# Optimization experiments

Measured on AMD Instinct MI355X. Metric: run time of the kernel, lower is better.

The kernel has to match this reference:

```python
import jax, jax.numpy as jnp
import numpy as np

EMB = 768
HEADS = 12
HEAD_DIM = EMB // HEADS
LN_EPS = 1e-5


def _layernorm(x, g, b):
    mu = jnp.mean(x, axis=-1, keepdims=True)
    var = jnp.mean(jnp.square(x - mu), axis=-1, keepdims=True)
    return (x - mu) * jax.lax.rsqrt(var + LN_EPS) * g + b


def _att_block(x, ln_g, ln_b, w_qkv, b_qkv, w_proj, b_proj):
    # x: [b, n, e]
    B, N, E = x.shape
    h, d = HEADS, HEAD_DIM
    qkv = _layernorm(x, ln_g, ln_b) @ w_qkv.T + b_qkv          # [b, n, 3e]
    # einops 'b n (h d qkv)': last axis factors as (h, d, 3), qkv innermost
    qkv = qkv.reshape(B, N, h, d, 3)
    qkv = jnp.moveaxis(qkv, (4, 2), (0, 2))                    # [3, b, h, n, d]
    q, k, v = qkv[0], qkv[1], qkv[2]
    scale = d ** (-0.5)
    # NOTE: original code DIVIDES by scale (= multiplies by sqrt(d)) -- faithful
    scores = jnp.einsum('bhqd,bhkd->bhqk', q, k) / scale       # [b, h, n, n]
    attn = jax.nn.softmax(scores, axis=-1)
    out = jnp.einsum('bhqk,bhkd->bhqd', attn, v)               # [b, h, n, d]
    out = out.transpose(0, 2, 1, 3).reshape(B, N, E)           # [b, n, e]
    return x + out @ w_proj.T + b_proj


def setup_inputs() -> dict:
    key = jax.random.key(0)
    ks = jax.random.split(key, 8)
    B, N, E = 2, 2048, EMB
    s = E ** (-0.5)
    return {
        'modal1': jax.random.normal(ks[0], (B, N, E), jnp.float32),
        'modal2': jax.random.normal(ks[1], (B, N, E), jnp.float32),
        'ln1_g': jnp.ones((E,), jnp.float32),
        'ln1_b': jnp.zeros((E,), jnp.float32),
        'w_qkv1': jax.random.normal(ks[2], (3 * E, E), jnp.float32) * s,
        'b_qkv1': jnp.zeros((3 * E,), jnp.float32),
        'w_proj1': jax.random.normal(ks[3], (E, E), jnp.float32) * s,
        'b_proj1': jnp.zeros((E,), jnp.float32),
        'ln2_g': jnp.ones((E,), jnp.float32),
        'ln2_b': jnp.zeros((E,), jnp.float32),
        'w_qkv2': jax.random.normal(ks[4], (3 * E, E), jnp.float32) * s,
        'b_qkv2': jnp.zeros((3 * E,), jnp.float32),
        'w_proj2': jax.random.normal(ks[5], (E, E), jnp.float32) * s,
        'b_proj2': jnp.zeros((E,), jnp.float32),
    }


def reference(modal1, modal2, ln1_g, ln1_b, w_qkv1, b_qkv1, w_proj1, b_proj1,
              ln2_g, ln2_b, w_qkv2, b_qkv2, w_proj2, b_proj2):
    out1 = _att_block(modal1, ln1_g, ln1_b, w_qkv1, b_qkv1, w_proj1, b_proj1)
    out2 = _att_block(modal2, ln2_g, ln2_b, w_qkv2, b_qkv2, w_proj2, b_proj2)
    return (out1, out2)
```

## Files before the change

### kernel.cpp

```cpp
#include <hip/hip_runtime.h>
#include <hip/hip_bf16.h>


typedef unsigned short u16;
typedef unsigned int   u32;
typedef __attribute__((ext_vector_type(4)))  float floatx4;
typedef __attribute__((ext_vector_type(16))) float floatx16;
typedef __attribute__((ext_vector_type(8)))  short shortx8;
typedef __attribute__((ext_vector_type(2)))  unsigned int uintx2;

#define EMB   768
#define SEQ   2048
#define NHEAD 12
#define HDIM  64
#define RPM   4096
#define NROW  8192
#define NUNIT 48
#define KTS   4096

__device__ __forceinline__ float bf2f(u16 h) {
  union { u32 u; float f; } v; v.u = ((u32)h) << 16; return v.f;
}
__device__ __forceinline__ u16 f2bf(float f) {
  union { float f; u32 u; } v; v.f = f;
  u32 r = v.u + 0x7fffu + ((v.u >> 16) & 1u);
  return (u16)(r >> 16);
}
__device__ __forceinline__ u32 cvtpk_bf16(float a, float b) {
  u32 r;
  asm("v_cvt_pk_bf16_f32 %0, %1, %2" : "=v"(r) : "v"(a), "v"(b));
  return r;
}
__device__ __forceinline__ void swap_halves(u32 a, u32 b, u32& x, u32& y) {
#if __has_builtin(__builtin_amdgcn_permlane32_swap)
  uintx2 r = __builtin_amdgcn_permlane32_swap(a, b, false, false);
  x = r.x; y = r.y;
#else
  u32 ax = (u32)__shfl_xor((int)a, 32);
  u32 bx = (u32)__shfl_xor((int)b, 32);
  bool h = (threadIdx.x & 32) != 0;
  x = h ? bx : a;
  y = h ? b : ax;
#endif
}

__global__ __launch_bounds__(256) void prep_wq(
    const float* __restrict__ wq1, const float* __restrict__ wq2,
    u16* __restrict__ wh, u16* __restrict__ wl)
{
  int bx = blockIdx.x;
  int modal = bx / 2304, rowp = bx % 2304;
  int typ = rowp / 768, hd = rowp % 768;
  const float* W = (modal ? wq2 : wq1) + (size_t)(hd * 3 + typ) * EMB;
  size_t dst = (size_t)bx * EMB;
  int t = threadIdx.x;
  #pragma unroll
  for (int i = 0; i < 3; ++i) {
    int e = t + i * 256;
    float v = W[e];
    u16 h = f2bf(v);
    wh[dst + e] = h;
    wl[dst + e] = f2bf(v - bf2f(h));
  }
}

__global__ __launch_bounds__(256) void prep_wp(
    const float* __restrict__ wp1, const float* __restrict__ wp2,
    u16* __restrict__ wh)
{
  int bx = blockIdx.x;
  int modal = bx / 768, row = bx % 768;
  const float* W = (modal ? wp2 : wp1) + (size_t)row * EMB;
  size_t dst = (size_t)bx * EMB;
  int t = threadIdx.x;
  #pragma unroll
  for (int i = 0; i < 3; ++i) {
    int e = t + i * 256;
    wh[dst + e] = f2bf(W[e]);
  }
}

__global__ __launch_bounds__(256) void k_ln(
    const float* __restrict__ x1, const float* __restrict__ x2,
    const float* __restrict__ g1, const float* __restrict__ b1,
    const float* __restrict__ g2, const float* __restrict__ b2,
    u16* __restrict__ xn_hi, u16* __restrict__ xn_lo)
{
  int row = blockIdx.x;
  int modal = row >> 12;
  const float* x = modal ? x2 : x1;
  const float* g = modal ? g2 : g1;
  const float* bb = modal ? b2 : b1;
  int r = row & (RPM - 1);
  const float* xr = x + (size_t)r * EMB;
  int t = threadIdx.x;
  float v0 = xr[t], v1 = xr[t + 256], v2 = xr[t + 512];
  float s = v0 + v1 + v2;
  float s2 = v0 * v0 + v1 * v1 + v2 * v2;
  #pragma unroll
  for (int m = 1; m < 64; m <<= 1) { s += __shfl_xor(s, m); s2 += __shfl_xor(s2, m); }
  __shared__ float ls[4], ls2[4];
  int w = t >> 6;
  if ((t & 63) == 0) { ls[w] = s; ls2[w] = s2; }
  __syncthreads();
  s = ls[0] + ls[1] + ls[2] + ls[3];
  s2 = ls2[0] + ls2[1] + ls2[2] + ls2[3];
  float mu = s * (1.0f / EMB);
  float var = s2 * (1.0f / EMB) - mu * mu;
  float rs = rsqrtf(var + 1e-5f);
  size_t base = (size_t)row * EMB;
  float vv[3] = { v0, v1, v2 };
  #pragma unroll
  for (int i = 0; i < 3; ++i) {
    int e = t + i * 256;
    float xn = (vv[i] - mu) * rs * g[e] + bb[e];
    u16 h = f2bf(xn);
    xn_hi[base + e] = h;
    xn_lo[base + e] = f2bf(xn - bf2f(h));
  }
}

__global__ __launch_bounds__(256) void k_qkv(
    const u16* __restrict__ xn_hi, const u16* __restrict__ xn_lo,
    const u16* __restrict__ wqh, const u16* __restrict__ wql,
    const float* __restrict__ bq1, const float* __restrict__ bq2,
    u16* __restrict__ q_hi, u16* __restrict__ q_lo,
    u16* __restrict__ k_hi, u16* __restrict__ k_lo,
    u16* __restrict__ vT)
{
  int mt = blockIdx.x, ntile = blockIdx.y, modal = blockIdx.z;
  const float* BQ = modal ? bq2 : bq1;
  int typ = ntile / 6;
  int hd0 = (ntile % 6) * 128;

  __shared__ __align__(16) u16 As_hi[128 * 32], Wh[128 * 32], As_lo[128 * 32], Wl[128 * 32];

  int tid = threadIdx.x, lane = tid & 63, w = tid >> 6;
  int wm = (w >> 1) * 64, wn = (w & 1) * 64;
  int lc = lane & 15, lq = lane >> 4;

  int srow = lane >> 2;
  int schunk = ((lane & 3) ^ (srow & 3)) << 3;

  floatx4 acc[4][4] = {};
  const u16* aH = xn_hi + (size_t)(modal * RPM + mt * 128) * EMB;
  const u16* aL = xn_lo + (size_t)(modal * RPM + mt * 128) * EMB;
  const u16* wH = wqh + (size_t)(modal * 2304 + typ * 768 + hd0) * EMB;
  const u16* wL = wql + (size_t)(modal * 2304 + typ * 768 + hd0) * EMB;

  for (int k0 = 0; k0 < EMB; k0 += 32) {
    if (typ != 2) {
      #pragma unroll
      for (int c = 0; c < 8; ++c) {
        int seg = w * 8 + c;
        int tile = seg >> 3, segin = seg & 7;
        size_t off = (size_t)(segin * 16 + srow) * EMB + k0 + schunk;
        const u16* src; u16* dstb;
        if (tile == 0)      { src = aH + off; dstb = As_hi; }
        else if (tile == 1) { src = wH + off; dstb = Wh; }
        else if (tile == 2) { src = aL + off; dstb = As_lo; }
        else                { src = wL + off; dstb = Wl; }
        __builtin_amdgcn_global_load_lds(
            (const __attribute__((address_space(1))) unsigned int*)src,
            (__attribute__((address_space(3))) unsigned int*)(dstb + segin * 512), 16, 0, 0);
      }
    } else {
      #pragma unroll
      for (int c = 0; c < 4; ++c) {
        int seg = w * 4 + c;
        int tile = seg >> 3, segin = seg & 7;
        size_t off = (size_t)(segin * 16 + srow) * EMB + k0 + schunk;
        const u16* src; u16* dstb;
        if (tile == 0) { src = aH + off; dstb = As_hi; }
        else           { src = wH + off; dstb = Wh; }
        __builtin_amdgcn_global_load_lds(
            (const __attribute__((address_space(1))) unsigned int*)src,
            (__attribute__((address_space(3))) unsigned int*)(dstb + segin * 512), 16, 0, 0);
      }
    }
    __syncthreads();

    shortx8 ah[4], al[4], whf[4], wlf[4];
    int rsw = lc & 3;
    int ca = (lq ^ rsw) << 3;
    #pragma unroll
    for (int i = 0; i < 4; ++i) {
      int ra = wm + i * 16 + lc, rw = wn + i * 16 + lc;
      ah[i]  = *(const shortx8*)&As_hi[ra * 32 + ca];
      whf[i] = *(const shortx8*)&Wh[rw * 32 + ca];
      if (typ != 2) {
        al[i]  = *(const shortx8*)&As_lo[ra * 32 + ca];
        wlf[i] = *(const shortx8*)&Wl[rw * 32 + ca];
      }
    }
    #pragma unroll
    for (int i = 0; i < 4; ++i)
      #pragma unroll
      for (int jn = 0; jn < 4; ++jn) {
        acc[i][jn] = __builtin_amdgcn_mfma_f32_16x16x32_bf16(ah[i], whf[jn], acc[i][jn], 0, 0, 0);
        if (typ != 2) {
          acc[i][jn] = __builtin_amdgcn_mfma_f32_16x16x32_bf16(al[i], whf[jn], acc[i][jn], 0, 0, 0);
          acc[i][jn] = __builtin_amdgcn_mfma_f32_16x16x32_bf16(ah[i], wlf[jn], acc[i][jn], 0, 0, 0);
        }
      }
    __syncthreads();
  }

  #pragma unroll
  for (int i = 0; i < 4; ++i) {
    int mrow0 = mt * 128 + wm + i * 16 + lq * 4;
    #pragma unroll
    for (int jn = 0; jn < 4; ++jn) {
      int colp = hd0 + wn + jn * 16 + lc;
      int h = colp >> 6, d = colp & 63;
      float bias = BQ[colp * 3 + typ];
      #pragma unroll
      for (int r = 0; r < 4; ++r) {
        int mrow = mrow0 + r;
        int b = mrow >> 11, nq = mrow & (SEQ - 1);
        int uu = modal * 24 + b * 12 + h;
        float val = acc[i][jn][r] + bias;
        if (typ == 0) {
          size_t o = ((size_t)uu * SEQ + nq) * HDIM + d;
          u16 hh = f2bf(val); q_hi[o] = hh; q_lo[o] = f2bf(val - bf2f(hh));
        } else if (typ == 1) {
          size_t o = ((size_t)uu * SEQ + nq) * HDIM + d;
          u16 hh = f2bf(val); k_hi[o] = hh; k_lo[o] = f2bf(val - bf2f(hh));
        } else {
          vT[((size_t)uu * HDIM + d) * SEQ + nq] = f2bf(val);
        }
      }
    }
  }
}

__global__ __launch_bounds__(256, 3) void k_attn(
    const u16* __restrict__ q_hi, const u16* __restrict__ q_lo,
    const u16* __restrict__ k_hi, const u16* __restrict__ k_lo,
    const u16* __restrict__ vT, u16* __restrict__ attn_out)
{
  int id = blockIdx.x + (blockIdx.y << 4);
  int xcd = id & 7, j = id >> 3;
  int u = xcd * 6 + (j >> 4);
  int qt = j & 15;

  __shared__ __align__(16) u16 lds[2][3 * KTS];

  int tid = threadIdx.x, lane = tid & 63, w = tid >> 6;
  int col = lane & 31, hi = lane >> 5;
  int swz = (col & 7) << 4;

  shortx8 qh[4], qlo[4];
  {
    size_t qb = ((size_t)u * SEQ + qt * 128 + w * 32 + col) * HDIM + hi * 8;
    #pragma unroll
    for (int s = 0; s < 4; ++s) {
      qh[s]  = *(const shortx8*)(q_hi + qb + s * 16);
      qlo[s] = *(const shortx8*)(q_lo + qb + s * 16);
    }
  }

  int lrow = lane >> 3;
  int lcol = ((lane & 7) ^ lrow) << 3;
  const u16* kh_src = k_hi + (size_t)u * SEQ * HDIM;
  const u16* kl_src = k_lo + (size_t)u * SEQ * HDIM;
  const u16* v_src  = vT  + (size_t)u * HDIM * SEQ;

  auto stage = [&](int buf, int kc) {
    #pragma unroll
    for (int c = 0; c < 6; ++c) {
      int seg = w * 6 + c;
      int tile = seg >> 3, segin = seg & 7;
      u16* dst = &lds[buf][tile * KTS + segin * 512];
      const u16* src;
      if (tile == 0)      src = kh_src + (size_t)(kc + segin * 8 + lrow) * HDIM + lcol;
      else if (tile == 1) src = kl_src + (size_t)(kc + segin * 8 + lrow) * HDIM + lcol;
      else                src = v_src  + (size_t)(segin * 8 + lrow) * SEQ + kc + lcol;
      __builtin_amdgcn_global_load_lds(
          (const __attribute__((address_space(1))) unsigned int*)src,
          (__attribute__((address_space(3))) unsigned int*)dst, 16, 0, 0);
    }
  };

  floatx16 O0 = {}, O1 = {};
  float m_r = -1e30f, lsum = 0.0f;
  const float Cs = 11.5415603271f;
  const float THR = 8.0f;

  stage(0, 0);
  __syncthreads();

  for (int t = 0; t < SEQ / 64; ++t) {
    int cur = t & 1;
    if (t + 1 < SEQ / 64) stage(cur ^ 1, (t + 1) * 64);

    const char* Kh = (const char*)&lds[cur][0];
    const char* Kl = (const char*)&lds[cur][KTS];
    const char* Vt = (const char*)&lds[cur][2 * KTS];

    floatx16 S0 = {}, S1 = {};
    __builtin_amdgcn_s_setprio(1);
    #pragma unroll
    for (int s = 0; s < 4; ++s) {
      int cb = (s * 32 + hi * 16) ^ swz;
      shortx8 kf0 = *(const shortx8*)(Kh + col * 128 + cb);
      shortx8 kl0 = *(const shortx8*)(Kl + col * 128 + cb);
      shortx8 kf1 = *(const shortx8*)(Kh + (32 + col) * 128 + cb);
      shortx8 kl1 = *(const shortx8*)(Kl + (32 + col) * 128 + cb);
      S0 = __builtin_amdgcn_mfma_f32_32x32x16_bf16(kf0, qh[s],  S0, 0, 0, 0);
      S1 = __builtin_amdgcn_mfma_f32_32x32x16_bf16(kf1, qh[s],  S1, 0, 0, 0);
      S0 = __builtin_amdgcn_mfma_f32_32x32x16_bf16(kf0, qlo[s], S0, 0, 0, 0);
      S1 = __builtin_amdgcn_mfma_f32_32x32x16_bf16(kf1, qlo[s], S1, 0, 0, 0);
      S0 = __builtin_amdgcn_mfma_f32_32x32x16_bf16(kl0, qh[s],  S0, 0, 0, 0);
      S1 = __builtin_amdgcn_mfma_f32_32x32x16_bf16(kl1, qh[s],  S1, 0, 0, 0);
    }
    __builtin_amdgcn_s_setprio(0);

    float tm[16];
    #pragma unroll
    for (int r = 0; r < 16; ++r) tm[r] = fmaxf(S0[r], S1[r]);
    #pragma unroll
    for (int st = 8; st >= 1; st >>= 1)
      #pragma unroll
      for (int i = 0; i < st; ++i) tm[i] = fmaxf(tm[i], tm[i + st]);
    float mx = tm[0] * Cs;
    mx = fmaxf(mx, __shfl_xor(mx, 32));

    if (!__all(mx <= m_r + THR)) {
      float mn = fmaxf(m_r, mx);
      float alpha = __builtin_amdgcn_exp2f(m_r - mn);
      m_r = mn;
      lsum *= alpha;
      #pragma unroll
      for (int r = 0; r < 16; ++r) {
        int qsrc = (r & 3) + 8 * (r >> 2) + 4 * hi;
        union { float f; int i; } a; a.f = alpha;
        a.i = __builtin_amdgcn_ds_bpermute(qsrc << 2, a.i);
        O0[r] *= a.f; O1[r] *= a.f;
      }
    }

    #pragma unroll
    for (int r = 0; r < 16; ++r) {
      S0[r] = __builtin_amdgcn_exp2f(fmaf(Cs, S0[r], -m_r));
      S1[r] = __builtin_amdgcn_exp2f(fmaf(Cs, S1[r], -m_r));
    }
    #pragma unroll
    for (int r = 0; r < 16; ++r) tm[r] = S0[r] + S1[r];
    #pragma unroll
    for (int st = 8; st >= 1; st >>= 1)
      #pragma unroll
      for (int i = 0; i < st; ++i) tm[i] += tm[i + st];
    lsum += tm[0];

    shortx8 pf[4];
    #pragma unroll
    for (int kt = 0; kt < 2; ++kt)
      #pragma unroll
      for (int h2 = 0; h2 < 2; ++h2) {
        floatx16 Sv = kt ? S1 : S0;
        int b0 = h2 * 8;
        u32 A = cvtpk_bf16(Sv[b0 + 0], Sv[b0 + 1]);
        u32 B = cvtpk_bf16(Sv[b0 + 2], Sv[b0 + 3]);
        u32 C = cvtpk_bf16(Sv[b0 + 4], Sv[b0 + 5]);
        u32 D = cvtpk_bf16(Sv[b0 + 6], Sv[b0 + 7]);
        u32 w0, w1, w2, w3;
        swap_halves(A, C, w0, w2);
        swap_halves(B, D, w1, w3);
        union { u32 uu[4]; shortx8 ss; } pk_;
        pk_.uu[0] = w0; pk_.uu[1] = w1; pk_.uu[2] = w2; pk_.uu[3] = w3;
        pf[kt * 2 + h2] = pk_.ss;
      }

    __builtin_amdgcn_s_setprio(1);
    #pragma unroll
    for (int ks = 0; ks < 4; ++ks) {
      int cb = (ks * 32 + hi * 16) ^ swz;
      shortx8 v0 = *(const shortx8*)(Vt + col * 128 + cb);
      shortx8 v1 = *(const shortx8*)(Vt + (32 + col) * 128 + cb);
      O0 = __builtin_amdgcn_mfma_f32_32x32x16_bf16(pf[ks], v0, O0, 0, 0, 0);
      O1 = __builtin_amdgcn_mfma_f32_32x32x16_bf16(pf[ks], v1, O1, 0, 0, 0);
    }
    __builtin_amdgcn_s_setprio(0);

    __syncthreads();
  }

  float lt = lsum + __shfl_xor(lsum, 32);
  float rl = __builtin_amdgcn_rcpf(lt);
  int modal = u / 24, b = (u / 12) & 1, h = u % 12;
  size_t obase = ((size_t)(modal * RPM + b * SEQ + qt * 128 + w * 32)) * EMB + h * 64 + col;
  #pragma unroll
  for (int r = 0; r < 16; ++r) {
    int ql_ = (r & 3) + 8 * (r >> 2) + 4 * hi;
    union { float f; int i; } a; a.f = rl;
    a.i = __builtin_amdgcn_ds_bpermute(ql_ << 2, a.i);
    size_t ob = obase + (size_t)ql_ * EMB;
    attn_out[ob]      = f2bf(O0[r] * a.f);
    attn_out[ob + 32] = f2bf(O1[r] * a.f);
  }
}

__global__ __launch_bounds__(256) void k_proj(
    const u16* __restrict__ ao, const u16* __restrict__ wph,
    const float* __restrict__ x1, const float* __restrict__ x2,
    const float* __restrict__ bp1, const float* __restrict__ bp2,
    float* __restrict__ out)
{
  int mt = blockIdx.x, ntile = blockIdx.y, modal = blockIdx.z;
  const float* BP = modal ? bp2 : bp1;
  const float* x  = modal ? x2 : x1;

  __shared__ __align__(16) u16 As[64 * 32], Ws[128 * 32];
  int tid = threadIdx.x, lane = tid & 63, w = tid >> 6;
  int wm = (w >> 1) * 32, wn = (w & 1) * 64;
  int lc = lane & 15, lq = lane >> 4;

  int srow = lane >> 2;
  int schunk = ((lane & 3) ^ (srow & 3)) << 3;

  floatx4 acc[2][4] = {};
  const u16* aP = ao  + (size_t)(modal * RPM + mt * 64) * EMB;
  const u16* wP = wph + (size_t)(modal * 768 + ntile * 128) * EMB;

  for (int k0 = 0; k0 < EMB; k0 += 32) {
    #pragma unroll
    for (int c = 0; c < 3; ++c) {
      int seg = w * 3 + c;
      const u16* src; u16* dst;
      if (seg < 4) {
        src = aP + (size_t)(seg * 16 + srow) * EMB + k0 + schunk;
        dst = As + seg * 512;
      } else {
        int s2 = seg - 4;
        src = wP + (size_t)(s2 * 16 + srow) * EMB + k0 + schunk;
        dst = Ws + s2 * 512;
      }
      __builtin_amdgcn_global_load_lds(
          (const __attribute__((address_space(1))) unsigned int*)src,
          (__attribute__((address_space(3))) unsigned int*)dst, 16, 0, 0);
    }
    __syncthreads();

    int ca = (lq ^ (lc & 3)) << 3;
    shortx8 af[2], wf[4];
    #pragma unroll
    for (int i = 0; i < 2; ++i) af[i] = *(const shortx8*)&As[(wm + i * 16 + lc) * 32 + ca];
    #pragma unroll
    for (int i = 0; i < 4; ++i) wf[i] = *(const shortx8*)&Ws[(wn + i * 16 + lc) * 32 + ca];
    #pragma unroll
    for (int i = 0; i < 2; ++i)
      #pragma unroll
      for (int jn = 0; jn < 4; ++jn)
        acc[i][jn] = __builtin_amdgcn_mfma_f32_16x16x32_bf16(af[i], wf[jn], acc[i][jn], 0, 0, 0);
    __syncthreads();
  }

  #pragma unroll
  for (int i = 0; i < 2; ++i) {
    int mrow0 = mt * 64 + wm + i * 16 + lq * 4;
    #pragma unroll
    for (int jn = 0; jn < 4; ++jn) {
      int col = ntile * 128 + wn + jn * 16 + lc;
      float bias = BP[col];
      #pragma unroll
      for (int r = 0; r < 4; ++r) {
        int mrow = mrow0 + r;
        float val = acc[i][jn][r] + bias + x[(size_t)mrow * EMB + col];
        out[((size_t)(modal * RPM + mrow)) * EMB + col] = val;
      }
    }
  }
}

extern "C" void kernel_launch(void* const* d_in, const int* in_sizes, int n_in,
                              void* d_out, int out_size, void* d_ws, size_t ws_size,
                              hipStream_t stream) {
  const float* modal1 = (const float*)d_in[0];
  const float* modal2 = (const float*)d_in[1];
  const float* ln1_g  = (const float*)d_in[2];
  const float* ln1_b  = (const float*)d_in[3];
  const float* w_qkv1 = (const float*)d_in[4];
  const float* b_qkv1 = (const float*)d_in[5];
  const float* w_proj1= (const float*)d_in[6];
  const float* b_proj1= (const float*)d_in[7];
  const float* ln2_g  = (const float*)d_in[8];
  const float* ln2_b  = (const float*)d_in[9];
  const float* w_qkv2 = (const float*)d_in[10];
  const float* b_qkv2 = (const float*)d_in[11];
  const float* w_proj2= (const float*)d_in[12];
  const float* b_proj2= (const float*)d_in[13];
  float* out = (float*)d_out;

  const size_t BUFE = (size_t)NROW * EMB;
  const size_t WQE  = (size_t)2 * 2304 * EMB;
  u16* xn_hi = (u16*)d_ws;
  u16* xn_lo = xn_hi + BUFE;
  u16* q_hi  = xn_lo + BUFE;
  u16* q_lo  = q_hi + BUFE;
  u16* k_hi  = q_lo + BUFE;
  u16* k_lo  = k_hi + BUFE;
  u16* vT    = k_lo + BUFE;
  u16* wq_h  = vT + BUFE;
  u16* wq_l  = wq_h + WQE;
  u16* attn  = xn_hi;
  u16* wp_h  = q_lo;

  prep_wq<<<4608, 256, 0, stream>>>(w_qkv1, w_qkv2, wq_h, wq_l);
  k_ln<<<NROW, 256, 0, stream>>>(modal1, modal2, ln1_g, ln1_b, ln2_g, ln2_b, xn_hi, xn_lo);
  dim3 g2(32, 18, 2);
  k_qkv<<<g2, 256, 0, stream>>>(xn_hi, xn_lo, wq_h, wq_l, b_qkv1, b_qkv2,
                                q_hi, q_lo, k_hi, k_lo, vT);
  dim3 g3(16, 48);
  k_attn<<<g3, 256, 0, stream>>>(q_hi, q_lo, k_hi, k_lo, vT, attn);
  prep_wp<<<1536, 256, 0, stream>>>(w_proj1, w_proj2, wp_h);
  dim3 g4(64, 6, 2);
  k_proj<<<g4, 256, 0, stream>>>(attn, wp_h, modal1, modal2, b_proj1, b_proj2, out);
}
```

Measured before the change: 355.5 us.

## Double-buffer QKV and proj GEMM staging; compute softmax row sums via MFMA

The QKV and output-projection GEMMs now double-buffer their LDS tiles. The next K-slice is issued with global_load_lds before the current one is computed, and partial vmcnt waits with raw barriers replace __syncthreads, so global latency overlaps MFMA work. In attention, exp2 and bf16 packing are interleaved per k-step with the PV MFMAs. The softmax denominator is accumulated by an extra MFMA against a ones vector, which removes the scalar sum reduction and the final bpermute. The cost is doubled LDS in the GEMMs (lower occupancy) and an extra MFMA per PV step, plus denominators summed from bf16-rounded probabilities.

New measurement: 387.2 us. +8.9%, slower.

```diff
diff --git a/kernel.cpp b/kernel.cpp
--- a/kernel.cpp
+++ b/kernel.cpp
@@ -133,7 +133,8 @@
   int typ = ntile / 6;
   int hd0 = (ntile % 6) * 128;
 
-  __shared__ __align__(16) u16 As_hi[128 * 32], Wh[128 * 32], As_lo[128 * 32], Wl[128 * 32];
+  __shared__ __align__(16) u16 As_hi[2][128 * 32], Wh[2][128 * 32],
+                               As_lo[2][128 * 32], Wl[2][128 * 32];
 
   int tid = threadIdx.x, lane = tid & 63, w = tid >> 6;
   int wm = (w >> 1) * 64, wn = (w & 1) * 64;
@@ -148,7 +149,7 @@
   const u16* wH = wqh + (size_t)(modal * 2304 + typ * 768 + hd0) * EMB;
   const u16* wL = wql + (size_t)(modal * 2304 + typ * 768 + hd0) * EMB;
 
-  for (int k0 = 0; k0 < EMB; k0 += 32) {
+  auto stage = [&](int buf, int k0) {
     if (typ != 2) {
       #pragma unroll
       for (int c = 0; c < 8; ++c) {
@@ -156,10 +157,10 @@
         int tile = seg >> 3, segin = seg & 7;
         size_t off = (size_t)(segin * 16 + srow) * EMB + k0 + schunk;
         const u16* src; u16* dstb;
-        if (tile == 0)      { src = aH + off; dstb = As_hi; }
-        else if (tile == 1) { src = wH + off; dstb = Wh; }
-        else if (tile == 2) { src = aL + off; dstb = As_lo; }
-        else                { src = wL + off; dstb = Wl; }
+        if (tile == 0)      { src = aH + off; dstb = &As_hi[buf][0]; }
+        else if (tile == 1) { src = wH + off; dstb = &Wh[buf][0]; }
+        else if (tile == 2) { src = aL + off; dstb = &As_lo[buf][0]; }
+        else                { src = wL + off; dstb = &Wl[buf][0]; }
         __builtin_amdgcn_global_load_lds(
             (const __attribute__((address_space(1))) unsigned int*)src,
             (__attribute__((address_space(3))) unsigned int*)(dstb + segin * 512), 16, 0, 0);
@@ -171,14 +172,29 @@
         int tile = seg >> 3, segin = seg & 7;
         size_t off = (size_t)(segin * 16 + srow) * EMB + k0 + schunk;
         const u16* src; u16* dstb;
-        if (tile == 0) { src = aH + off; dstb = As_hi; }
-        else           { src = wH + off; dstb = Wh; }
+        if (tile == 0) { src = aH + off; dstb = &As_hi[buf][0]; }
+        else           { src = wH + off; dstb = &Wh[buf][0]; }
         __builtin_amdgcn_global_load_lds(
             (const __attribute__((address_space(1))) unsigned int*)src,
             (__attribute__((address_space(3))) unsigned int*)(dstb + segin * 512), 16, 0, 0);
       }
     }
-    __syncthreads();
+  };
+
+  stage(0, 0);
+  for (int kk = 0; kk < 24; ++kk) {
+    int cur = kk & 1;
+    bool more = (kk + 1 < 24);
+    if (more) stage(cur ^ 1, (kk + 1) * 32);
+    if (typ != 2) {
+      if (more) asm volatile("s_waitcnt vmcnt(8)" ::: "memory");
+      else      asm volatile("s_waitcnt vmcnt(0)" ::: "memory");
+    } else {
+      if (more) asm volatile("s_waitcnt vmcnt(4)" ::: "memory");
+      else      asm volatile("s_waitcnt vmcnt(0)" ::: "memory");
+    }
+    __builtin_amdgcn_s_barrier();
+    __builtin_amdgcn_sched_barrier(0);
 
     shortx8 ah[4], al[4], whf[4], wlf[4];
     int rsw = lc & 3;
@@ -186,11 +202,11 @@
     #pragma unroll
     for (int i = 0; i < 4; ++i) {
       int ra = wm + i * 16 + lc, rw = wn + i * 16 + lc;
-      ah[i]  = *(const shortx8*)&As_hi[ra * 32 + ca];
-      whf[i] = *(const shortx8*)&Wh[rw * 32 + ca];
+      ah[i]  = *(const shortx8*)&As_hi[cur][ra * 32 + ca];
+      whf[i] = *(const shortx8*)&Wh[cur][rw * 32 + ca];
       if (typ != 2) {
-        al[i]  = *(const shortx8*)&As_lo[ra * 32 + ca];
-        wlf[i] = *(const shortx8*)&Wl[rw * 32 + ca];
+        al[i]  = *(const shortx8*)&As_lo[cur][ra * 32 + ca];
+        wlf[i] = *(const shortx8*)&Wl[cur][rw * 32 + ca];
       }
     }
     #pragma unroll
@@ -203,7 +219,9 @@
           acc[i][jn] = __builtin_amdgcn_mfma_f32_16x16x32_bf16(ah[i], wlf[jn], acc[i][jn], 0, 0, 0);
         }
       }
-    __syncthreads();
+    asm volatile("s_waitcnt lgkmcnt(0)" ::: "memory");
+    __builtin_amdgcn_s_barrier();
+    __builtin_amdgcn_sched_barrier(0);
   }
 
   #pragma unroll
@@ -282,8 +300,13 @@
     }
   };
 
+  shortx8 ONES;
+  #pragma unroll
+  for (int i = 0; i < 8; ++i) ONES[i] = (short)0x3F80;
+
   floatx16 O0 = {}, O1 = {};
-  float m_r = -1e30f, lsum = 0.0f;
+  floatx16 Osum = {};
+  float m_r = -1e30f;
   const float Cs = 11.5415603271f;
   const float THR = 8.0f;
 
@@ -316,88 +339,68 @@
     }
     __builtin_amdgcn_s_setprio(0);
 
-    float tm[16];
-    #pragma unroll
-    for (int r = 0; r < 16; ++r) tm[r] = fmaxf(S0[r], S1[r]);
-    #pragma unroll
-    for (int st = 8; st >= 1; st >>= 1)
-      #pragma unroll
-      for (int i = 0; i < st; ++i) tm[i] = fmaxf(tm[i], tm[i + st]);
-    float mx = tm[0] * Cs;
+    float pm[16];
+    #pragma unroll
+    for (int r = 0; r < 16; ++r) pm[r] = fmaxf(S0[r], S1[r]);
+    float g0 = fmaxf(fmaxf(pm[0],  pm[1]),  pm[2]);
+    float g1 = fmaxf(fmaxf(pm[3],  pm[4]),  pm[5]);
+    float g2 = fmaxf(fmaxf(pm[6],  pm[7]),  pm[8]);
+    float g3 = fmaxf(fmaxf(pm[9],  pm[10]), pm[11]);
+    float g4 = fmaxf(fmaxf(pm[12], pm[13]), pm[14]);
+    float mx = fmaxf(fmaxf(fmaxf(g0, g1), g2), fmaxf(fmaxf(g3, g4), pm[15])) * Cs;
     mx = fmaxf(mx, __shfl_xor(mx, 32));
 
     if (!__all(mx <= m_r + THR)) {
       float mn = fmaxf(m_r, mx);
       float alpha = __builtin_amdgcn_exp2f(m_r - mn);
       m_r = mn;
-      lsum *= alpha;
       #pragma unroll
       for (int r = 0; r < 16; ++r) {
         int qsrc = (r & 3) + 8 * (r >> 2) + 4 * hi;
         union { float f; int i; } a; a.f = alpha;
         a.i = __builtin_amdgcn_ds_bpermute(qsrc << 2, a.i);
-        O0[r] *= a.f; O1[r] *= a.f;
-      }
-    }
-
-    #pragma unroll
-    for (int r = 0; r < 16; ++r) {
-      S0[r] = __builtin_amdgcn_exp2f(fmaf(Cs, S0[r], -m_r));
-      S1[r] = __builtin_amdgcn_exp2f(fmaf(Cs, S1[r], -m_r));
-    }
-    #pragma unroll
-    for (int r = 0; r < 16; ++r) tm[r] = S0[r] + S1[r];
-    #pragma unroll
-    for (int st = 8; st >= 1; st >>= 1)
-      #pragma unroll
-      for (int i = 0; i < st; ++i) tm[i] += tm[i + st];
-    lsum += tm[0];
-
-    shortx8 pf[4];
-    #pragma unroll
-    for (int kt = 0; kt < 2; ++kt)
-      #pragma unroll
-      for (int h2 = 0; h2 < 2; ++h2) {
-        floatx16 Sv = kt ? S1 : S0;
-        int b0 = h2 * 8;
-        u32 A = cvtpk_bf16(Sv[b0 + 0], Sv[b0 + 1]);
-        u32 B = cvtpk_bf16(Sv[b0 + 2], Sv[b0 + 3]);
-        u32 C = cvtpk_bf16(Sv[b0 + 4], Sv[b0 + 5]);
-        u32 D = cvtpk_bf16(Sv[b0 + 6], Sv[b0 + 7]);
-        u32 w0, w1, w2, w3;
-        swap_halves(A, C, w0, w2);
-        swap_halves(B, D, w1, w3);
-        union { u32 uu[4]; shortx8 ss; } pk_;
-        pk_.uu[0] = w0; pk_.uu[1] = w1; pk_.uu[2] = w2; pk_.uu[3] = w3;
-        pf[kt * 2 + h2] = pk_.ss;
-      }
-
-    __builtin_amdgcn_s_setprio(1);
+        O0[r] *= a.f; O1[r] *= a.f; Osum[r] *= a.f;
+      }
+    }
+
     #pragma unroll
     for (int ks = 0; ks < 4; ++ks) {
+      const int h2 = ks & 1;
+      float ee[8];
+      #pragma unroll
+      for (int i = 0; i < 8; ++i) {
+        float sv = (ks < 2) ? S0[h2 * 8 + i] : S1[h2 * 8 + i];
+        ee[i] = __builtin_amdgcn_exp2f(fmaf(Cs, sv, -m_r));
+      }
+      u32 A = cvtpk_bf16(ee[0], ee[1]);
+      u32 B = cvtpk_bf16(ee[2], ee[3]);
+      u32 C = cvtpk_bf16(ee[4], ee[5]);
+      u32 D = cvtpk_bf16(ee[6], ee[7]);
+      u32 w0, w1, w2, w3;
+      swap_halves(A, C, w0, w2);
+      swap_halves(B, D, w1, w3);
+      union { u32 uu[4]; shortx8 ss; } pk_;
+      pk_.uu[0] = w0; pk_.uu[1] = w1; pk_.uu[2] = w2; pk_.uu[3] = w3;
       int cb = (ks * 32 + hi * 16) ^ swz;
       shortx8 v0 = *(const shortx8*)(Vt + col * 128 + cb);
       shortx8 v1 = *(const shortx8*)(Vt + (32 + col) * 128 + cb);
-      O0 = __builtin_amdgcn_mfma_f32_32x32x16_bf16(pf[ks], v0, O0, 0, 0, 0);
-      O1 = __builtin_amdgcn_mfma_f32_32x32x16_bf16(pf[ks], v1, O1, 0, 0, 0);
-    }
-    __builtin_amdgcn_s_setprio(0);
+      O0   = __builtin_amdgcn_mfma_f32_32x32x16_bf16(pk_.ss, v0,   O0,   0, 0, 0);
+      O1   = __builtin_amdgcn_mfma_f32_32x32x16_bf16(pk_.ss, v1,   O1,   0, 0, 0);
+      Osum = __builtin_amdgcn_mfma_f32_32x32x16_bf16(pk_.ss, ONES, Osum, 0, 0, 0);
+    }
 
     __syncthreads();
   }
 
-  float lt = lsum + __shfl_xor(lsum, 32);
-  float rl = __builtin_amdgcn_rcpf(lt);
   int modal = u / 24, b = (u / 12) & 1, h = u % 12;
   size_t obase = ((size_t)(modal * RPM + b * SEQ + qt * 128 + w * 32)) * EMB + h * 64 + col;
   #pragma unroll
   for (int r = 0; r < 16; ++r) {
     int ql_ = (r & 3) + 8 * (r >> 2) + 4 * hi;
-    union { float f; int i; } a; a.f = rl;
-    a.i = __builtin_amdgcn_ds_bpermute(ql_ << 2, a.i);
+    float rl = __builtin_amdgcn_rcpf(Osum[r]);
     size_t ob = obase + (size_t)ql_ * EMB;
-    attn_out[ob]      = f2bf(O0[r] * a.f);
-    attn_out[ob + 32] = f2bf(O1[r] * a.f);
+    attn_out[ob]      = f2bf(O0[r] * rl);
+    attn_out[ob + 32] = f2bf(O1[r] * rl);
   }
 }
 
@@ -411,7 +414,7 @@
   const float* BP = modal ? bp2 : bp1;
   const float* x  = modal ? x2 : x1;
 
-  __shared__ __align__(16) u16 As[64 * 32], Ws[128 * 32];
+  __shared__ __align__(16) u16 As[2][64 * 32], Ws[2][128 * 32];
   int tid = threadIdx.x, lane = tid & 63, w = tid >> 6;
   int wm = (w >> 1) * 32, wn = (w & 1) * 64;
   int lc = lane & 15, lq = lane >> 4;
@@ -423,37 +426,49 @@
   const u16* aP = ao  + (size_t)(modal * RPM + mt * 64) * EMB;
   const u16* wP = wph + (size_t)(modal * 768 + ntile * 128) * EMB;
 
-  for (int k0 = 0; k0 < EMB; k0 += 32) {
+  auto stage = [&](int buf, int k0) {
     #pragma unroll
     for (int c = 0; c < 3; ++c) {
       int seg = w * 3 + c;
       const u16* src; u16* dst;
       if (seg < 4) {
         src = aP + (size_t)(seg * 16 + srow) * EMB + k0 + schunk;
-        dst = As + seg * 512;
+        dst = &As[buf][0] + seg * 512;
       } else {
         int s2 = seg - 4;
         src = wP + (size_t)(s2 * 16 + srow) * EMB + k0 + schunk;
-        dst = Ws + s2 * 512;
+        dst = &Ws[buf][0] + s2 * 512;
       }
       __builtin_amdgcn_global_load_lds(
           (const __attribute__((address_space(1))) unsigned int*)src,
           (__attribute__((address_space(3))) unsigned int*)dst, 16, 0, 0);
     }
-    __syncthreads();
+  };
+
+  stage(0, 0);
+  for (int kk = 0; kk < 24; ++kk) {
+    int cur = kk & 1;
+    bool more = (kk + 1 < 24);
+    if (more) stage(cur ^ 1, (kk + 1) * 32);
+    if (more) asm volatile("s_waitcnt vmcnt(3)" ::: "memory");
+    else      asm volatile("s_waitcnt vmcnt(0)" ::: "memory");
+    __builtin_amdgcn_s_barrier();
+    __builtin_amdgcn_sched_barrier(0);
 
     int ca = (lq ^ (lc & 3)) << 3;
     shortx8 af[2], wf[4];
     #pragma unroll
-    for (int i = 0; i < 2; ++i) af[i] = *(const shortx8*)&As[(wm + i * 16 + lc) * 32 + ca];
-    #pragma unroll
-    for (int i = 0; i < 4; ++i) wf[i] = *(const shortx8*)&Ws[(wn + i * 16 + lc) * 32 + ca];
+    for (int i = 0; i < 2; ++i) af[i] = *(const shortx8*)&As[cur][(wm + i * 16 + lc) * 32 + ca];
+    #pragma unroll
+    for (int i = 0; i < 4; ++i) wf[i] = *(const shortx8*)&Ws[cur][(wn + i * 16 + lc) * 32 + ca];
     #pragma unroll
     for (int i = 0; i < 2; ++i)
       #pragma unroll
       for (int jn = 0; jn < 4; ++jn)
         acc[i][jn] = __builtin_amdgcn_mfma_f32_16x16x32_bf16(af[i], wf[jn], acc[i][jn], 0, 0, 0);
-    __syncthreads();
+    asm volatile("s_waitcnt lgkmcnt(0)" ::: "memory");
+    __builtin_amdgcn_s_barrier();
+    __builtin_amdgcn_sched_barrier(0);
   }
 
   #pragma unroll
```
